# Optimization experiments

Hardware: AMD Instinct MI355X
Metric: run time of the kernel (lower is better)

The kernel has to match this reference:

```python
import jax, jax.numpy as jnp
import numpy as np

K = 8        # num_caps
NITER = 3    # routing iterations per layer
NLAYER = 2   # number of NeibRoutLayer layers
TAU = 1.0
SLOPE = 0.01 # torch leaky_relu default
EPS = 1e-12  # torch F.normalize default eps


def capsnorm(v, k):
    # L2-normalize each of k capsule chunks along its delta_d axis.
    n, d = v.shape
    vk = v.reshape(n, k, d // k)
    nr = jnp.sqrt(jnp.sum(vk * vk, axis=2, keepdims=True))
    return (vk / jnp.maximum(nr, EPS)).reshape(n, d)


def rout(x, src, trg, k, niter, tau):
    n, d = x.shape
    dd = d // k
    x = capsnorm(x, k)
    z = x[src].reshape(-1, k, dd)  # [m, k, dd] neighbor capsules (constant over iters)
    u = x
    for _ in range(niter):
        # per-edge, per-capsule agreement score
        p = jnp.einsum('mkc,mkc->mk', z, u[trg].reshape(-1, k, dd))
        p = jax.nn.softmax(p / tau, axis=1)
        msg = (z * p[:, :, None]).reshape(-1, d)
        u = jax.ops.segment_sum(msg, trg, num_segments=n) + x
        u = capsnorm(u, k)
    return u


def setup_inputs() -> dict:
    key = jax.random.key(0)
    k1, k2, k3, k4 = jax.random.split(key, 4)
    n, m, in_dim, hid = 50000, 500000, 500, 64
    x = jax.random.normal(k1, (n, in_dim), dtype=jnp.float32)
    src_trg = jax.random.randint(k2, (2, m), 0, n)
    stdv = 1.0 / np.sqrt(hid)  # SparseInputLinear.reset_parameters
    W = jax.random.uniform(k3, (in_dim, hid), minval=-stdv, maxval=stdv, dtype=jnp.float32)
    b = jax.random.uniform(k4, (hid,), minval=-stdv, maxval=stdv, dtype=jnp.float32)
    return {"x": x, "src_trg": src_trg, "W": W, "b": b}


def reference(x, src_trg, W, b):
    # eval mode: dropout(p=0.0, training=False) is identity
    src, trg = src_trg[0], src_trg[1]
    h = jax.nn.leaky_relu(x @ W + b, negative_slope=SLOPE)
    for _ in range(NLAYER):
        h = jax.nn.leaky_relu(rout(h, src, trg, K, NITER, TAU), negative_slope=SLOPE)
    return h
```

## Files before the change

kernel.cpp:

```cpp
#include <hip/hip_runtime.h>
#include <hip/hip_bf16.h>

static constexpr float SLOPE = 0.01f;
static constexpr float EPSN  = 1e-12f;

typedef float f32x4 __attribute__((ext_vector_type(4)));
typedef short short8 __attribute__((ext_vector_type(8)));

#define KPAD 512
#define PREP_BLOCKS (KPAD * 64 / 256)

template <int CTRL>
__device__ __forceinline__ float dpp_add(float x) {
  const int y = __builtin_amdgcn_mov_dpp(__builtin_bit_cast(int, x), CTRL, 0xF, 0xF, true);
  return x + __builtin_bit_cast(float, y);
}

__device__ __forceinline__ void bf16_split(float v, short& hi, short& lo) {
  __hip_bfloat16 h = __float2bfloat16(v);
  float hf = __bfloat162float(h);
  __hip_bfloat16 l = __float2bfloat16(v - hf);
  hi = __builtin_bit_cast(short, h);
  lo = __builtin_bit_cast(short, l);
}

__device__ __forceinline__ void load_lds16(const float* g, float* l) {
  __builtin_amdgcn_global_load_lds(
      (const __attribute__((address_space(1))) unsigned int*)g,
      (__attribute__((address_space(3))) unsigned int*)l, 16, 0, 0);
}

__global__ __launch_bounds__(256) void prep_hist_k(
    const float* __restrict__ W, short* __restrict__ w2h,
    short* __restrict__ w2l, float* __restrict__ zbuf, int in_dim,
    const int* __restrict__ trg, int* __restrict__ counts, int m) {
  if ((int)blockIdx.x < PREP_BLOCKS) {
    const int idx = blockIdx.x * 256 + threadIdx.x;
    if (idx < 4) zbuf[idx] = 0.0f;
    if (idx >= KPAD * 64) return;
    const int k = idx >> 6, col = idx & 63;
    const float v = (k < in_dim) ? W[(size_t)k * 64 + col] : 0.0f;
    short hi, lo;
    bf16_split(v, hi, lo);
    const int kt = k >> 5, kc = (k >> 3) & 3, e = k & 7;
    const int off = (((kt * 4 + kc) * 64) + col) * 8 + e;
    w2h[off] = hi;
    w2l[off] = lo;
  } else {
    const int e = (blockIdx.x - PREP_BLOCKS) * 256 + threadIdx.x;
    if (e < m) atomicAdd(&counts[trg[e]], 1);
  }
}

__device__ __forceinline__ void stage_tile(const float* __restrict__ x,
                                           const float* __restrict__ zbuf,
                                           float* ldsbuf, int row0w, int kt,
                                           int n, int in_dim, int lane) {
  const int rl = lane >> 4;
  const int gl = lane & 15;
#pragma unroll
  for (int i = 0; i < 4; ++i) {
    const int r    = i * 4 + rl;
    const int gsrc = gl ^ (r & 7);
    const int k    = kt * 64 + gsrc * 4;
    int grow = row0w + r;
    grow = grow < n ? grow : n - 1;
    const float* src = (k + 4 <= in_dim) ? (x + (size_t)grow * in_dim + k) : zbuf;
    load_lds16(src, ldsbuf + i * 256);
  }
}

__global__ __launch_bounds__(256) void gemm_scatter_k(
    const float* __restrict__ x, const short* __restrict__ w2h,
    const short* __restrict__ w2l, const float* __restrict__ b,
    const float* __restrict__ zbuf, float* __restrict__ xn, int n, int in_dim,
    const int* __restrict__ src, const int* __restrict__ trg,
    int* __restrict__ cursor, int* __restrict__ src_sorted, int m,
    int gemm_blocks) {
  __shared__ __align__(16) float xs[4][2][1024];

  if ((int)blockIdx.x >= gemm_blocks) {
    const int e = (blockIdx.x - gemm_blocks) * 256 + threadIdx.x;
    if (e < m) {
      const int pos = atomicAdd(&cursor[trg[e]], 1);
      src_sorted[pos] = src[e];
    }
    return;
  }

  const int tid   = threadIdx.x;
  const int lane  = tid & 63;
  const int w     = tid >> 6;
  const int l15   = lane & 15;
  const int kcL   = lane >> 4;
  const int row0  = blockIdx.x * 64;
  const int row0w = row0 + w * 16;
  const int sw4   = l15 & 7;

  f32x4 acc0 = {0.f, 0.f, 0.f, 0.f};
  f32x4 acc1 = {0.f, 0.f, 0.f, 0.f};
  f32x4 acc2 = {0.f, 0.f, 0.f, 0.f};
  f32x4 acc3 = {0.f, 0.f, 0.f, 0.f};

  stage_tile(x, zbuf, &xs[w][0][0], row0w, 0, n, in_dim, lane);

  for (int kt = 0; kt < 8; ++kt) {
    float* cur = &xs[w][kt & 1][0];
    float* nxt = &xs[w][(kt & 1) ^ 1][0];

    const int s00 = ((kcL * 2)     ^ sw4) * 4;
    const int s01 = ((kcL * 2 + 1) ^ sw4) * 4;
    const int s10 = ((8 + kcL * 2)     ^ sw4) * 4;
    const int s11 = ((8 + kcL * 2 + 1) ^ sw4) * 4;
    const float4 fa0 = *reinterpret_cast<const float4*>(&cur[l15 * 64 + s00]);
    const float4 fb0 = *reinterpret_cast<const float4*>(&cur[l15 * 64 + s01]);
    const float4 fa1 = *reinterpret_cast<const float4*>(&cur[l15 * 64 + s10]);
    const float4 fb1 = *reinterpret_cast<const float4*>(&cur[l15 * 64 + s11]);

    if (kt < 7) stage_tile(x, zbuf, nxt, row0w, kt + 1, n, in_dim, lane);

#pragma unroll
    for (int ks = 0; ks < 2; ++ks) {
      const float4 A0 = ks ? fa1 : fa0;
      const float4 A1 = ks ? fb1 : fb0;
      short hb[8], lb[8];
      bf16_split(A0.x, hb[0], lb[0]);
      bf16_split(A0.y, hb[1], lb[1]);
      bf16_split(A0.z, hb[2], lb[2]);
      bf16_split(A0.w, hb[3], lb[3]);
      bf16_split(A1.x, hb[4], lb[4]);
      bf16_split(A1.y, hb[5], lb[5]);
      bf16_split(A1.z, hb[6], lb[6]);
      bf16_split(A1.w, hb[7], lb[7]);
      const short8 ah = *reinterpret_cast<const short8*>(hb);
      const short8 al = *reinterpret_cast<const short8*>(lb);
      const int ktg = kt * 2 + ks;
      const size_t base = ((size_t)(ktg * 4 + kcL) * 64) * 8;
#pragma unroll
      for (int nt = 0; nt < 4; ++nt) {
        const short8 bh = *reinterpret_cast<const short8*>(w2h + base + (size_t)(nt * 16 + l15) * 8);
        const short8 bl = *reinterpret_cast<const short8*>(w2l + base + (size_t)(nt * 16 + l15) * 8);
        f32x4& acc = nt == 0 ? acc0 : nt == 1 ? acc1 : nt == 2 ? acc2 : acc3;
        acc = __builtin_amdgcn_mfma_f32_16x16x32_bf16(ah, bh, acc, 0, 0, 0);
        acc = __builtin_amdgcn_mfma_f32_16x16x32_bf16(ah, bl, acc, 0, 0, 0);
        acc = __builtin_amdgcn_mfma_f32_16x16x32_bf16(al, bh, acc, 0, 0, 0);
      }
    }
  }

#pragma unroll
  for (int nt = 0; nt < 4; ++nt) {
    const f32x4 acc = nt == 0 ? acc0 : nt == 1 ? acc1 : nt == 2 ? acc2 : acc3;
    const float bcol = b[nt * 16 + l15];
#pragma unroll
    for (int reg = 0; reg < 4; ++reg) {
      float v = acc[reg] + bcol;
      v = v > 0.f ? v : SLOPE * v;
      float s = v * v;
      s = dpp_add<0xB1>(s);
      s = dpp_add<0x4E>(s);
      s += __shfl_xor(s, 4);
      const float inv = 1.0f / fmaxf(sqrtf(s), EPSN);
      const int grow = row0 + w * 16 + ((lane >> 4) << 2) + reg;
      if (grow < n) xn[(size_t)grow * 64 + nt * 16 + l15] = v * inv;
    }
  }
}

__global__ __launch_bounds__(256) void scanA_k(const int* __restrict__ counts,
                                               int* __restrict__ bsum, int n) {
  const int i = blockIdx.x * 256 + threadIdx.x;
  int v = (i < n) ? counts[i] : 0;
  v += __shfl_xor(v, 1);  v += __shfl_xor(v, 2);  v += __shfl_xor(v, 4);
  v += __shfl_xor(v, 8);  v += __shfl_xor(v, 16); v += __shfl_xor(v, 32);
  __shared__ int wsum[4];
  if ((threadIdx.x & 63) == 0) wsum[threadIdx.x >> 6] = v;
  __syncthreads();
  if (threadIdx.x == 0) bsum[blockIdx.x] = wsum[0] + wsum[1] + wsum[2] + wsum[3];
}

__global__ __launch_bounds__(256) void scanB_k(int* __restrict__ bsum, int nblk,
                                               int* __restrict__ row_ptr, int n, int m) {
  const int i = threadIdx.x;
  const int lane = i & 63;
  const int wave = i >> 6;
  const int v = (i < nblk) ? bsum[i] : 0;
  int inc = v;
#pragma unroll
  for (int d = 1; d < 64; d <<= 1) {
    int t = __shfl_up(inc, d);
    if (lane >= d) inc += t;
  }
  __shared__ int wsum[4];
  if (lane == 63) wsum[wave] = inc;
  __syncthreads();
  int base = 0;
  for (int q = 0; q < wave; ++q) base += wsum[q];
  if (i < nblk) bsum[i] = base + inc - v;
  if (i == 0) row_ptr[n] = m;
}

__global__ __launch_bounds__(256) void scanC_k(const int* __restrict__ counts,
                                               const int* __restrict__ bsum,
                                               int* __restrict__ row_ptr,
                                               int* __restrict__ cursor, int n) {
  const int i = blockIdx.x * 256 + threadIdx.x;
  const int lane = threadIdx.x & 63;
  const int wave = threadIdx.x >> 6;
  const int v = (i < n) ? counts[i] : 0;
  int inc = v;
#pragma unroll
  for (int d = 1; d < 64; d <<= 1) {
    int t = __shfl_up(inc, d);
    if (lane >= d) inc += t;
  }
  __shared__ int wsum[4];
  if (lane == 63) wsum[wave] = inc;
  __syncthreads();
  int base = bsum[blockIdx.x];
  for (int q = 0; q < wave; ++q) base += wsum[q];
  const int excl = base + inc - v;
  if (i < n) { row_ptr[i] = excl; cursor[i] = excl; }
}

template <int MODE>
__global__ __launch_bounds__(256) void rout_layer_k(
    const int* __restrict__ row_ptr, const int* __restrict__ src_sorted,
    const float* __restrict__ xn, float* __restrict__ dst, int n) {
  const int wid  = blockIdx.x * 4 + (threadIdx.x >> 6);
  const int lane = threadIdx.x & 63;
  if (wid >= n) return;
  const int g = lane >> 4;
  const int q = lane & 15;
  const size_t rowj = (size_t)wid * 64 + q * 4;
  const float4 fz = make_float4(0.f, 0.f, 0.f, 0.f);

  const float4 xj = *reinterpret_cast<const float4*>(xn + rowj);
  float u0 = xj.x, u1 = xj.y, u2 = xj.z, u3 = xj.w;

  const int e0  = row_ptr[wid];
  const int end = row_ptr[wid + 1];
  const int ntile = (end - e0 + 3) >> 2;

  const int eA = e0 + g, eB = eA + 4, eC = eA + 8, eD = eA + 12;
  const bool vA = eA < end, vB = eB < end, vC = eC < end, vD = eD < end;
  const int iA = vA ? src_sorted[eA] : wid;
  const int iB = vB ? src_sorted[eB] : wid;
  const int iC = vC ? src_sorted[eC] : wid;
  const int iD = vD ? src_sorted[eD] : wid;
  float4 zA = *reinterpret_cast<const float4*>(xn + (size_t)iA * 64 + q * 4);
  float4 zB = *reinterpret_cast<const float4*>(xn + (size_t)iB * 64 + q * 4);
  float4 zC = *reinterpret_cast<const float4*>(xn + (size_t)iC * 64 + q * 4);
  float4 zD = *reinterpret_cast<const float4*>(xn + (size_t)iD * 64 + q * 4);
  if (!vA) zA = fz;
  if (!vB) zB = fz;
  if (!vC) zC = fz;
  if (!vD) zD = fz;

  for (int t = 0; t < 3; ++t) {
    float a0 = 0.f, a1 = 0.f, a2 = 0.f, a3 = 0.f;

#define EDGE_BODY(Z)                                                   \
    {                                                                  \
      float d = (Z).x * u0;                                            \
      d = fmaf((Z).y, u1, d);                                          \
      d = fmaf((Z).z, u2, d);                                          \
      d = fmaf((Z).w, u3, d);                                          \
      d = dpp_add<0xB1>(d);                     \
      const float ee = __expf(d);           \
      float sm = dpp_add<0x4E>(ee);          \
      sm = dpp_add<0x124>(sm);               \
      sm = dpp_add<0x128>(sm);               \
      const float wgt = ee * __builtin_amdgcn_rcpf(sm);                \
      a0 = fmaf((Z).x, wgt, a0);                                       \
      a1 = fmaf((Z).y, wgt, a1);                                       \
      a2 = fmaf((Z).z, wgt, a2);                                       \
      a3 = fmaf((Z).w, wgt, a3);                                       \
    }

    EDGE_BODY(zA)
    EDGE_BODY(zB)
    EDGE_BODY(zC)
    EDGE_BODY(zD)
    for (int it = 4; it < ntile; ++it) {
      const int e = e0 + it * 4 + g;
      const bool vv = e < end;
      const int ss = vv ? src_sorted[e] : wid;
      float4 z = *reinterpret_cast<const float4*>(xn + (size_t)ss * 64 + q * 4);
      if (!vv) z = fz;
      EDGE_BODY(z)
    }
#undef EDGE_BODY

    a0 += __shfl_xor(a0, 16); a0 += __shfl_xor(a0, 32);
    a1 += __shfl_xor(a1, 16); a1 += __shfl_xor(a1, 32);
    a2 += __shfl_xor(a2, 16); a2 += __shfl_xor(a2, 32);
    a3 += __shfl_xor(a3, 16); a3 += __shfl_xor(a3, 32);
    a0 += xj.x; a1 += xj.y; a2 += xj.z; a3 += xj.w;
    float ss = a0 * a0 + a1 * a1 + a2 * a2 + a3 * a3;
    ss = dpp_add<0xB1>(ss);
    const float inv = 1.0f / fmaxf(sqrtf(ss), EPSN);
    u0 = a0 * inv; u1 = a1 * inv; u2 = a2 * inv; u3 = a3 * inv;
  }

  float v0 = u0, v1 = u1, v2 = u2, v3 = u3;
  v0 = v0 > 0.f ? v0 : SLOPE * v0;
  v1 = v1 > 0.f ? v1 : SLOPE * v1;
  v2 = v2 > 0.f ? v2 : SLOPE * v2;
  v3 = v3 > 0.f ? v3 : SLOPE * v3;
  if (MODE == 1) {
    float s3 = v0 * v0 + v1 * v1 + v2 * v2 + v3 * v3;
    s3 = dpp_add<0xB1>(s3);
    const float inv3 = 1.0f / fmaxf(sqrtf(s3), EPSN);
    v0 *= inv3; v1 *= inv3; v2 *= inv3; v3 *= inv3;
  }
  if (g == 0) {
    *reinterpret_cast<float4*>(dst + rowj) = make_float4(v0, v1, v2, v3);
  }
}

extern "C" void kernel_launch(void* const* d_in, const int* in_sizes, int n_in,
                              void* d_out, int out_size, void* d_ws, size_t ws_size,
                              hipStream_t stream) {
  const float* x       = (const float*)d_in[0];
  const int*   src_trg = (const int*)d_in[1];
  const float* W       = (const float*)d_in[2];
  const float* b       = (const float*)d_in[3];

  const int hid    = in_sizes[3];
  const int in_dim = in_sizes[2] / hid;
  const int n      = in_sizes[0] / in_dim;
  const int m      = in_sizes[1] / 2;
  const int* src = src_trg;
  const int* trg = src_trg + m;

  const size_t n64 = (size_t)n * hid;
  float* xn_a = (float*)d_ws;
  float* xn_b = xn_a + n64;
  short* w2h  = (short*)(xn_b + n64);
  short* w2l  = w2h + KPAD * 64;
  float* zbuf = (float*)(w2l + KPAD * 64);
  int*   ip   = (int*)(zbuf + 4);
  int* counts     = ip;
  int* row_ptr    = counts + n;
  int* cursor     = row_ptr + n + 1;
  int* bsum       = cursor + n;
  const int nblk  = (n + 255) / 256;
  int* src_sorted = bsum + nblk;
  float* out = (float*)d_out;

  const int mg = (m + 255) / 256;
  const int gemm_blocks = (n + 63) / 64;

  hipMemsetAsync(counts, 0, (size_t)n * sizeof(int), stream);
  prep_hist_k<<<PREP_BLOCKS + mg, 256, 0, stream>>>(
      W, w2h, w2l, zbuf, in_dim, trg, counts, m);

  scanA_k<<<nblk, 256, 0, stream>>>(counts, bsum, n);
  scanB_k<<<1, 256, 0, stream>>>(bsum, nblk, row_ptr, n, m);
  scanC_k<<<nblk, 256, 0, stream>>>(counts, bsum, row_ptr, cursor, n);

  gemm_scatter_k<<<gemm_blocks + mg, 256, 0, stream>>>(
      x, w2h, w2l, b, zbuf, xn_a, n, in_dim,
      src, trg, cursor, src_sorted, m, gemm_blocks);

  const int rb = (n + 3) / 4;
  rout_layer_k<1><<<rb, 256, 0, stream>>>(row_ptr, src_sorted, xn_a, xn_b, n);
  rout_layer_k<2><<<rb, 256, 0, stream>>>(row_ptr, src_sorted, xn_b, out, n);
}
```

Baseline: 147.5 us.

## Stage whole K panel into LDS upfront and split scatter into own kernel

The GEMM kernel now issues all eight K-tile loads for its rows into a 128 KB LDS buffer up front instead of double-buffering one tile ahead, which puts more memory requests in flight per wave. The edge scatter that shared a launch with the GEMM moves into its own kernel. The larger LDS footprint cuts occupancy to about one block per CU, and the GEMM no longer overlaps with the scatter work.

```diff
diff --git a/kernel.cpp b/kernel.cpp
--- a/kernel.cpp
+++ b/kernel.cpp
@@ -52,41 +52,11 @@
   }
 }
 
-__device__ __forceinline__ void stage_tile(const float* __restrict__ x,
-                                           const float* __restrict__ zbuf,
-                                           float* ldsbuf, int row0w, int kt,
-                                           int n, int in_dim, int lane) {
-  const int rl = lane >> 4;
-  const int gl = lane & 15;
-#pragma unroll
-  for (int i = 0; i < 4; ++i) {
-    const int r    = i * 4 + rl;
-    const int gsrc = gl ^ (r & 7);
-    const int k    = kt * 64 + gsrc * 4;
-    int grow = row0w + r;
-    grow = grow < n ? grow : n - 1;
-    const float* src = (k + 4 <= in_dim) ? (x + (size_t)grow * in_dim + k) : zbuf;
-    load_lds16(src, ldsbuf + i * 256);
-  }
-}
-
-__global__ __launch_bounds__(256) void gemm_scatter_k(
+__global__ __launch_bounds__(256) void gemm_mfma_capsnorm_k(
     const float* __restrict__ x, const short* __restrict__ w2h,
     const short* __restrict__ w2l, const float* __restrict__ b,
-    const float* __restrict__ zbuf, float* __restrict__ xn, int n, int in_dim,
-    const int* __restrict__ src, const int* __restrict__ trg,
-    int* __restrict__ cursor, int* __restrict__ src_sorted, int m,
-    int gemm_blocks) {
-  __shared__ __align__(16) float xs[4][2][1024];
-
-  if ((int)blockIdx.x >= gemm_blocks) {
-    const int e = (blockIdx.x - gemm_blocks) * 256 + threadIdx.x;
-    if (e < m) {
-      const int pos = atomicAdd(&cursor[trg[e]], 1);
-      src_sorted[pos] = src[e];
-    }
-    return;
-  }
+    const float* __restrict__ zbuf, float* __restrict__ xn, int n, int in_dim) {
+  __shared__ __align__(16) float xs[4][8][1024];
 
   const int tid   = threadIdx.x;
   const int lane  = tid & 63;
@@ -97,27 +67,43 @@
   const int row0w = row0 + w * 16;
   const int sw4   = l15 & 7;
 
+  {
+    const int rl = lane >> 4;
+    const int gl = lane & 15;
+#pragma unroll
+    for (int i = 0; i < 4; ++i) {
+      const int r = i * 4 + rl;
+      int grow = row0w + r;
+      grow = grow < n ? grow : n - 1;
+      const float* xrow = x + (size_t)grow * in_dim;
+      const int gsrc = gl ^ (r & 7);
+#pragma unroll
+      for (int kt = 0; kt < 8; ++kt) {
+        const int k = kt * 64 + gsrc * 4;
+        const float* src = (k + 4 <= in_dim) ? (xrow + k) : zbuf;
+        load_lds16(src, &xs[w][kt][i * 256]);
+      }
+    }
+  }
+
   f32x4 acc0 = {0.f, 0.f, 0.f, 0.f};
   f32x4 acc1 = {0.f, 0.f, 0.f, 0.f};
   f32x4 acc2 = {0.f, 0.f, 0.f, 0.f};
   f32x4 acc3 = {0.f, 0.f, 0.f, 0.f};
 
-  stage_tile(x, zbuf, &xs[w][0][0], row0w, 0, n, in_dim, lane);
-
+  const int s00 = ((kcL * 2)         ^ sw4) * 4;
+  const int s01 = ((kcL * 2 + 1)     ^ sw4) * 4;
+  const int s10 = ((8 + kcL * 2)     ^ sw4) * 4;
+  const int s11 = ((8 + kcL * 2 + 1) ^ sw4) * 4;
+  const int rowoff = l15 * 64;
+
+#pragma unroll
   for (int kt = 0; kt < 8; ++kt) {
-    float* cur = &xs[w][kt & 1][0];
-    float* nxt = &xs[w][(kt & 1) ^ 1][0];
-
-    const int s00 = ((kcL * 2)     ^ sw4) * 4;
-    const int s01 = ((kcL * 2 + 1) ^ sw4) * 4;
-    const int s10 = ((8 + kcL * 2)     ^ sw4) * 4;
-    const int s11 = ((8 + kcL * 2 + 1) ^ sw4) * 4;
-    const float4 fa0 = *reinterpret_cast<const float4*>(&cur[l15 * 64 + s00]);
-    const float4 fb0 = *reinterpret_cast<const float4*>(&cur[l15 * 64 + s01]);
-    const float4 fa1 = *reinterpret_cast<const float4*>(&cur[l15 * 64 + s10]);
-    const float4 fb1 = *reinterpret_cast<const float4*>(&cur[l15 * 64 + s11]);
-
-    if (kt < 7) stage_tile(x, zbuf, nxt, row0w, kt + 1, n, in_dim, lane);
+    const float* cur = &xs[w][kt][0];
+    const float4 fa0 = *reinterpret_cast<const float4*>(&cur[rowoff + s00]);
+    const float4 fb0 = *reinterpret_cast<const float4*>(&cur[rowoff + s01]);
+    const float4 fa1 = *reinterpret_cast<const float4*>(&cur[rowoff + s10]);
+    const float4 fb1 = *reinterpret_cast<const float4*>(&cur[rowoff + s11]);
 
 #pragma unroll
     for (int ks = 0; ks < 2; ++ks) {
@@ -223,6 +209,17 @@
   if (i < n) { row_ptr[i] = excl; cursor[i] = excl; }
 }
 
+__global__ __launch_bounds__(256) void scatter_k(const int* __restrict__ src,
+                                                 const int* __restrict__ trg,
+                                                 int* __restrict__ cursor,
+                                                 int* __restrict__ src_sorted, int m) {
+  const int e = blockIdx.x * blockDim.x + threadIdx.x;
+  if (e < m) {
+    const int pos = atomicAdd(&cursor[trg[e]], 1);
+    src_sorted[pos] = src[e];
+  }
+}
+
 template <int MODE>
 __global__ __launch_bounds__(256) void rout_layer_k(
     const int* __restrict__ row_ptr, const int* __restrict__ src_sorted,
@@ -359,10 +356,10 @@
   scanA_k<<<nblk, 256, 0, stream>>>(counts, bsum, n);
   scanB_k<<<1, 256, 0, stream>>>(bsum, nblk, row_ptr, n, m);
   scanC_k<<<nblk, 256, 0, stream>>>(counts, bsum, row_ptr, cursor, n);
-
-  gemm_scatter_k<<<gemm_blocks + mg, 256, 0, stream>>>(
-      x, w2h, w2l, b, zbuf, xn_a, n, in_dim,
-      src, trg, cursor, src_sorted, m, gemm_blocks);
+  scatter_k<<<mg, 256, 0, stream>>>(src, trg, cursor, src_sorted, m);
+
+  gemm_mfma_capsnorm_k<<<gemm_blocks, 256, 0, stream>>>(
+      x, w2h, w2l, b, zbuf, xn_a, n, in_dim);
 
   const int rb = (n + 3) / 4;
   rout_layer_k<1><<<rb, 256, 0, stream>>>(row_ptr, src_sorted, xn_a, xn_b, n);
```

New measurement: 188.8 us. +28.0%, slower.
